# Optimization experiments

Measured on AMD Instinct MI355X. Metric: run time of the kernel, lower is better.

## Reference

```python
import jax, jax.numpy as jnp
import numpy as np

N_NODES = 100000
N_EDGES = 800000
F_IN = 16
F_OUT = 16
NB = 4          # basis terms per coordinate dimension (dims=[4,4] -> K=16)
OUTPUT_SCALING = 1.0 / 128.0


def hat_basis(u, n):
    """'linear' RBF: hat functions on [-1,1]. u: [E] -> [E, n]."""
    centers = jnp.linspace(-1.0, 1.0, n, dtype=u.dtype)   # [n]
    width = 2.0 / (n - 1)
    return jnp.maximum(0.0, 1.0 - jnp.abs(u[:, None] - centers[None, :]) / width)


def setup_inputs() -> dict:
    key = jax.random.key(0)
    k1, k2, k3, k4, k5 = jax.random.split(key, 5)
    x = jax.random.normal(k1, (N_NODES, F_IN), dtype=jnp.float32)
    edge_attr = jax.random.normal(k2, (N_EDGES, 2), dtype=jnp.float32) * 0.7
    # conv weight tensor: [K, F_in, F_out], xavier-ish scale with gain 1/sqrt(34)
    W = jax.random.normal(k3, (NB * NB, F_IN, F_OUT), dtype=jnp.float32) * (
        (1.0 / np.sqrt(34.0)) * np.sqrt(2.0 / (F_IN + F_OUT)))
    edge_index_i = jax.random.randint(k4, (N_EDGES,), 0, N_NODES, dtype=jnp.int64)
    edge_index_j = jax.random.randint(k5, (N_EDGES,), 0, N_NODES, dtype=jnp.int64)
    return {"x": x, "edge_attr": edge_attr, "W": W,
            "edge_index_i": edge_index_i, "edge_index_j": edge_index_j}


def reference(x, edge_attr, W, edge_index_i, edge_index_j):
    # --- process(): centerIgnore mask, clamp, cartesian mapping (identity) ---
    mask = edge_index_i != edge_index_j                      # [E]
    mapped = jnp.clip(edge_attr, -1.0, 1.0)                  # [E, 2]

    # --- tensor-product 'linear' basis evaluation: [E, K] ---
    bx = hat_basis(mapped[:, 0], NB)                         # [E, NB]
    by = hat_basis(mapped[:, 1], NB)                         # [E, NB]
    basis = (bx[:, :, None] * by[:, None, :]).reshape(mapped.shape[0], NB * NB)

    # --- continuous conv: gather, per-edge basis-weighted linear, scatter ---
    xj = x[edge_index_j]                                     # [E, F_in] gather
    u = jnp.einsum('ei,kio->eko', xj, W)                     # [E, K, F_out]
    msg = jnp.einsum('ek,eko->eo', basis, u)                 # [E, F_out]
    msg = jnp.where(mask[:, None], msg, jnp.zeros((), msg.dtype))
    out = jax.ops.segment_sum(msg, edge_index_i, num_segments=x.shape[0])
    return out * OUTPUT_SCALING
```

## Files before the change

kernel.cpp:

```cpp
#include <hip/hip_runtime.h>

#define N_NODES 100000
#define N_EDGES 800000
#define NBY    ((N_NODES + 255) / 256)
#define HBLK   ((N_EDGES + 255) / 256)
#define OVF_CAP 65536
#define GA     1000
#define CHUNK  800
#define NBINS  512
#define NPB    196
#define CAPB   2048
#define GB_T   1024
#define CURSTRIDE 64

__device__ __forceinline__ unsigned short f2bf(float f) {
    union { float f; unsigned u; } v; v.f = f;
    unsigned u = v.u;
    return (unsigned short)((u + 0x7FFFu + ((u >> 16) & 1u)) >> 16);
}
__device__ __forceinline__ float bflo(unsigned u) {
    union { unsigned u; float f; } v; v.u = u << 16; return v.f;
}
__device__ __forceinline__ float bfhi(unsigned u) {
    union { unsigned u; float f; } v; v.u = u & 0xFFFF0000u; return v.f;
}

__global__ __launch_bounds__(256) void bucket_build(
    const float* __restrict__ edge_attr,
    const int* __restrict__ ei, const int* __restrict__ ej,
    int* __restrict__ cursor, uint2* __restrict__ bkt,
    int* __restrict__ ovfCnt, int* __restrict__ ovf) {
    const int b = blockIdx.x;
    __shared__ int hist[NBINS];
    __shared__ unsigned rawA[CHUNK];
    __shared__ unsigned rawB[CHUNK];
    __shared__ short rawBin[CHUNK];
    const int tid = threadIdx.x;
    for (int k = tid; k < NBINS; k += 256) hist[k] = 0;
    __syncthreads();
    const int base = b * CHUNK;

    for (int i = 0; i < CHUNK; i += 256) {
        const int j = i + tid;
        if (j >= CHUNK) continue;
        const int e = base + j;
        short binS = -1;
        if (e < N_EDGES) {
            const int di = ei[e];
            const int sj = ej[e];
            if (di != sj) {
                const float2 ea = ((const float2*)edge_attr)[e];
                float ux = fminf(fmaxf(ea.x, -1.f), 1.f);
                float uy = fminf(fmaxf(ea.y, -1.f), 1.f);
                float tx = (ux + 1.f) * 1.5f;
                float ty = (uy + 1.f) * 1.5f;
                int kx0 = min((int)tx, 2);
                int ky0 = min((int)ty, 2);
                float fx = tx - (float)kx0;
                float fy = ty - (float)ky0;
                unsigned fx12 = (unsigned)(fx * 4095.f + 0.5f);
                unsigned fy12 = (unsigned)(fy * 4095.f + 0.5f);
                const int bin = di / NPB;
                const unsigned local = (unsigned)(di - bin * NPB);
                rawA[j] = (unsigned)(sj * 512 + (kx0 * 4 + ky0) * 32);
                rawB[j] = fx12 | (fy12 << 12) | (local << 24);
                binS = (short)bin;
                atomicAdd(&hist[bin], 1);
            }
        }
        rawBin[j] = binS;
    }
    __syncthreads();

    for (int k = tid; k < NBINS; k += 256) {
        const int c = hist[k];
        int g = 0;
        if (c > 0) g = atomicAdd(&cursor[k * CURSTRIDE], c);
        hist[k] = k * CAPB + g;
    }
    __syncthreads();

    for (int i = 0; i < CHUNK; i += 256) {
        const int j = i + tid;
        if (j >= CHUNK) continue;
        const int bin = rawBin[j];
        if (bin < 0) continue;
        const int s = atomicAdd(&hist[bin], 1);
        if (s - bin * CAPB < CAPB) {
            bkt[s] = make_uint2(rawA[j], rawB[j]);
        } else {
            const int o = atomicAdd(ovfCnt, 1);
            if (o < OVF_CAP) ovf[o] = base + j;
        }
    }
}

__global__ __launch_bounds__(GB_T) void gather_conv(
    const int* __restrict__ cursor, const uint2* __restrict__ bkt,
    const float* __restrict__ x, const float* __restrict__ W,
    float* __restrict__ out,
    const int* __restrict__ ovfCnt, const int* __restrict__ ovf,
    const float* __restrict__ edge_attr, const int* __restrict__ ei,
    const int* __restrict__ ej) {
    const int bin = blockIdx.x;
    const int tid = threadIdx.x;
    __shared__ uint2 sorted[CAPB];
    __shared__ __align__(16) char u_buf[20480];
    __shared__ int h[NPB];
    __shared__ int st[NPB], en[NPB], cur[NPB];
    __shared__ float tile[NPB * 16];
    uint2* raw = (uint2*)u_buf;
    float* Wl  = (float*)u_buf;

    for (int j = tid; j < NPB; j += GB_T) h[j] = 0;
    __syncthreads();

    const int cnt = min(cursor[bin * CURSTRIDE], CAPB);
    const int pad = (cnt + NPB <= CAPB) ? 1 : 0;
    const uint2* rb = bkt + (size_t)bin * CAPB;

    for (int p = tid; p < cnt; p += GB_T) {
        uint2 r = rb[p];
        raw[p] = r;
        atomicAdd(&h[r.y >> 24], 1);
    }
    __syncthreads();

    int c0 = (tid < NPB) ? h[tid] : 0;
    for (int off = 1; off < NPB; off <<= 1) {
        int tmp = 0;
        if (tid < NPB && tid >= off) tmp = h[tid - off];
        __syncthreads();
        if (tid < NPB) h[tid] += tmp;
        __syncthreads();
    }
    if (tid < NPB) {
        const int sh = tid * pad;
        en[tid]  = h[tid] + sh;
        st[tid]  = h[tid] - c0 + sh;
        cur[tid] = h[tid] - c0 + sh;
    }
    __syncthreads();

    for (int p = tid; p < cnt; p += GB_T) {
        uint2 r = raw[p];
        int pos = atomicAdd(&cur[r.y >> 24], 1);
        sorted[pos] = r;
    }
    __syncthreads();

    {
        float4 w = ((const float4*)W)[tid];
        const int k = tid >> 6, i = (tid >> 2) & 15, o4 = tid & 3;
        *(float4*)&Wl[k * 320 + i * 20 + o4 * 4] = w;
    }
    __syncthreads();

    const float U = 1.f / 4095.f;
    const float S = 1.f / 128.f;
    if (tid < 4 * NPB) {
        const int node = tid >> 2;
        const int q4 = tid & 3;
        float t[16][4];
#pragma unroll
        for (int k = 0; k < 16; ++k)
#pragma unroll
            for (int i = 0; i < 4; ++i) t[k][i] = 0.f;

        const int lo = st[node], hi2 = en[node];
        uint2 m = make_uint2(0u, 0u);
        float4 xv = make_float4(0.f, 0.f, 0.f, 0.f);
        if (lo < hi2) {
            m = sorted[lo];
            xv = ((const float4*)x)[(m.x >> 9) * 4 + q4];
        }
        for (int idx = lo; idx < hi2; ++idx) {
            const uint2 mc = m;
            const float4 xc = xv;
            if (idx + 1 < hi2) {
                m = sorted[idx + 1];
                xv = ((const float4*)x)[(m.x >> 9) * 4 + q4];
            }
            const unsigned koff = (mc.x >> 5) & 15u;
            const int kx0 = (int)(koff >> 2);
            const int ky0 = (int)(koff & 3u);
            const float fx = (float)(mc.y & 0xFFFu) * U;
            const float fy = (float)((mc.y >> 12) & 0xFFFu) * U;
            float wx[4], wy[4];
#pragma unroll
            for (int a = 0; a < 4; ++a) {
                wx[a] = (a == kx0) ? (1.f - fx) : ((a == kx0 + 1) ? fx : 0.f);
                wy[a] = (a == ky0) ? (1.f - fy) : ((a == ky0 + 1) ? fy : 0.f);
            }
            const float xr[4] = {xc.x, xc.y, xc.z, xc.w};
#pragma unroll
            for (int kx = 0; kx < 4; ++kx)
#pragma unroll
                for (int ky = 0; ky < 4; ++ky) {
                    const float w = wx[kx] * wy[ky];
#pragma unroll
                    for (int i = 0; i < 4; ++i)
                        t[kx * 4 + ky][i] = fmaf(w, xr[i], t[kx * 4 + ky][i]);
                }
        }

        float po[16];
#pragma unroll
        for (int o = 0; o < 16; ++o) po[o] = 0.f;
#pragma unroll
        for (int k = 0; k < 16; ++k)
#pragma unroll
            for (int il = 0; il < 4; ++il) {
                const float tv = t[k][il];
                const float4* wr = (const float4*)&Wl[k * 320 + (q4 * 4 + il) * 20];
                const float4 w0 = wr[0], w1 = wr[1], w2 = wr[2], w3 = wr[3];
                po[0]  = fmaf(tv, w0.x, po[0]);  po[1]  = fmaf(tv, w0.y, po[1]);
                po[2]  = fmaf(tv, w0.z, po[2]);  po[3]  = fmaf(tv, w0.w, po[3]);
                po[4]  = fmaf(tv, w1.x, po[4]);  po[5]  = fmaf(tv, w1.y, po[5]);
                po[6]  = fmaf(tv, w1.z, po[6]);  po[7]  = fmaf(tv, w1.w, po[7]);
                po[8]  = fmaf(tv, w2.x, po[8]);  po[9]  = fmaf(tv, w2.y, po[9]);
                po[10] = fmaf(tv, w2.z, po[10]); po[11] = fmaf(tv, w2.w, po[11]);
                po[12] = fmaf(tv, w3.x, po[12]); po[13] = fmaf(tv, w3.y, po[13]);
                po[14] = fmaf(tv, w3.z, po[14]); po[15] = fmaf(tv, w3.w, po[15]);
            }

#pragma unroll
        for (int o = 0; o < 16; ++o) {
            po[o] += __shfl_xor(po[o], 1);
            po[o] += __shfl_xor(po[o], 2);
        }
        if (q4 == 0) {
            float* tr = &tile[node * 16];
#pragma unroll
            for (int o = 0; o < 16; ++o) tr[o] = po[o] * S;
        }
    }
    __syncthreads();

    const int m = min(*ovfCnt, OVF_CAP);
    if (m > 0) {
        const int nlo = bin * NPB;
        const int nhi = min(nlo + NPB, N_NODES);
        for (int i = tid; i < m; i += GB_T) {
            const int e = ovf[i];
            const int di = ei[e];
            if (di < nlo || di >= nhi) continue;
            const int sj = ej[e];
            const float2 ea = ((const float2*)edge_attr)[e];
            float ux = fminf(fmaxf(ea.x, -1.f), 1.f);
            float uy = fminf(fmaxf(ea.y, -1.f), 1.f);
            float tx = (ux + 1.f) * 1.5f, ty = (uy + 1.f) * 1.5f;
            int kx0 = min((int)tx, 2), ky0 = min((int)ty, 2);
            float fx = tx - (float)kx0, fy = ty - (float)ky0;
            float wgt[4] = {(1.f-fx)*(1.f-fy)*S, (1.f-fx)*fy*S, fx*(1.f-fy)*S, fx*fy*S};
            int kidx[4] = {kx0*4+ky0, kx0*4+ky0+1, (kx0+1)*4+ky0, (kx0+1)*4+ky0+1};
            const float* xj = x + (size_t)sj * 16;
            float msg[16];
#pragma unroll
            for (int o = 0; o < 16; ++o) msg[o] = 0.f;
#pragma unroll
            for (int p = 0; p < 4; ++p) {
                const float* wk = Wl + kidx[p] * 320;
                for (int ii = 0; ii < 16; ++ii) {
                    float xw = xj[ii] * wgt[p];
#pragma unroll
                    for (int o = 0; o < 16; ++o)
                        msg[o] = fmaf(xw, wk[ii * 20 + o], msg[o]);
                }
            }
            float* tr = &tile[(di - nlo) * 16];
#pragma unroll
            for (int o = 0; o < 16; ++o) atomicAdd(tr + o, msg[o]);
        }
        __syncthreads();
    }

    const int base = bin * NPB * 16;
    const int lim = N_NODES * 16 - base;
    for (int j = tid; j < NPB * 16; j += GB_T)
        if (j < lim) out[base + j] = tile[j];
}

__global__ __launch_bounds__(256) void y_only_kernel(
    const float* __restrict__ x, const float* __restrict__ W,
    unsigned short* __restrict__ Y) {
    const int n = blockIdx.x * 256 + threadIdx.x;
    const int kbase = blockIdx.y * 4;
    if (n >= N_NODES) return;
    const float4* xv = (const float4*)(x + n * 16);
    float4 a = xv[0], b = xv[1], c = xv[2], d = xv[3];
    float xr[16] = {a.x,a.y,a.z,a.w, b.x,b.y,b.z,b.w,
                    c.x,c.y,c.z,c.w, d.x,d.y,d.z,d.w};
    float acc[4][16];
#pragma unroll
    for (int kk = 0; kk < 4; ++kk)
#pragma unroll
        for (int o = 0; o < 16; ++o) acc[kk][o] = 0.f;
#pragma unroll
    for (int i = 0; i < 16; ++i)
#pragma unroll
        for (int kk = 0; kk < 4; ++kk) {
            const float* wrow = W + ((kbase + kk) * 256 + i * 16);
#pragma unroll
            for (int o = 0; o < 16; ++o)
                acc[kk][o] = fmaf(xr[i], wrow[o], acc[kk][o]);
        }
    unsigned short* dst = Y + (size_t)n * 256 + kbase * 16;
#pragma unroll
    for (int kk = 0; kk < 4; ++kk) {
        unsigned pk[8];
#pragma unroll
        for (int q = 0; q < 8; ++q)
            pk[q] = (unsigned)f2bf(acc[kk][2*q]) | ((unsigned)f2bf(acc[kk][2*q+1]) << 16);
        uint4* p = (uint4*)(dst + kk * 16);
        p[0] = make_uint4(pk[0], pk[1], pk[2], pk[3]);
        p[1] = make_uint4(pk[4], pk[5], pk[6], pk[7]);
    }
}

__global__ __launch_bounds__(256) void edge_kernel(
    const float* __restrict__ edge_attr, const int* __restrict__ ei,
    const int* __restrict__ ej, const unsigned short* __restrict__ Y,
    float* __restrict__ out) {
    const int e = blockIdx.x * 256 + threadIdx.x;
    if (e >= N_EDGES) return;
    const int di = ei[e];
    const int sj = ej[e];
    const float2 ea = ((const float2*)edge_attr)[e];
    if (di == sj) return;
    float ux = fminf(fmaxf(ea.x, -1.f), 1.f);
    float uy = fminf(fmaxf(ea.y, -1.f), 1.f);
    float tx = (ux + 1.f) * 1.5f;
    float ty = (uy + 1.f) * 1.5f;
    int kx0 = min((int)tx, 2);
    int ky0 = min((int)ty, 2);
    float fx = tx - (float)kx0;
    float fy = ty - (float)ky0;
    const float S = 1.f / 128.f;
    float w00 = (1.f - fx) * (1.f - fy) * S;
    float w01 = (1.f - fx) * fy * S;
    float w10 = fx * (1.f - fy) * S;
    float w11 = fx * fy * S;
    const unsigned short* base = Y + (size_t)sj * 256 + (kx0 * 4 + ky0) * 16;
    const uint4* pA = (const uint4*)base;
    const uint4* pB = (const uint4*)(base + 64);
    uint4 a0 = pA[0], a1 = pA[1], a2 = pA[2], a3 = pA[3];
    uint4 b0 = pB[0], b1 = pB[1], b2 = pB[2], b3 = pB[3];
    unsigned ra0[8] = {a0.x,a0.y,a0.z,a0.w, a1.x,a1.y,a1.z,a1.w};
    unsigned ra1[8] = {a2.x,a2.y,a2.z,a2.w, a3.x,a3.y,a3.z,a3.w};
    unsigned rb0[8] = {b0.x,b0.y,b0.z,b0.w, b1.x,b1.y,b1.z,b1.w};
    unsigned rb1[8] = {b2.x,b2.y,b2.z,b2.w, b3.x,b3.y,b3.z,b3.w};
    float* o16 = out + (size_t)di * 16;
#pragma unroll
    for (int q = 0; q < 8; ++q) {
        float m0 = bflo(ra0[q]) * w00 + bflo(ra1[q]) * w01
                 + bflo(rb0[q]) * w10 + bflo(rb1[q]) * w11;
        float m1 = bfhi(ra0[q]) * w00 + bfhi(ra1[q]) * w01
                 + bfhi(rb0[q]) * w10 + bfhi(rb1[q]) * w11;
        atomicAdd(o16 + 2 * q, m0);
        atomicAdd(o16 + 2 * q + 1, m1);
    }
}

__global__ __launch_bounds__(256) void edge_direct(
    const float* __restrict__ x, const float* __restrict__ edge_attr,
    const float* __restrict__ W, const int* __restrict__ ei,
    const int* __restrict__ ej, float* __restrict__ out) {
    const int e = blockIdx.x * 256 + threadIdx.x;
    if (e >= N_EDGES) return;
    const int di = ei[e];
    const int sj = ej[e];
    const float2 ea = ((const float2*)edge_attr)[e];
    if (di == sj) return;
    float ux = fminf(fmaxf(ea.x, -1.f), 1.f);
    float uy = fminf(fmaxf(ea.y, -1.f), 1.f);
    float tx = (ux + 1.f) * 1.5f, ty = (uy + 1.f) * 1.5f;
    int kx0 = min((int)tx, 2), ky0 = min((int)ty, 2);
    float fx = tx - (float)kx0, fy = ty - (float)ky0;
    const float S = 1.f / 128.f;
    float wgt[4] = {(1.f-fx)*(1.f-fy)*S, (1.f-fx)*fy*S, fx*(1.f-fy)*S, fx*fy*S};
    int kidx[4] = {kx0*4+ky0, kx0*4+ky0+1, (kx0+1)*4+ky0, (kx0+1)*4+ky0+1};
    const float* xj = x + (size_t)sj * 16;
    float xr[16];
#pragma unroll
    for (int i = 0; i < 16; ++i) xr[i] = xj[i];
    float msg[16];
#pragma unroll
    for (int o = 0; o < 16; ++o) msg[o] = 0.f;
#pragma unroll
    for (int p = 0; p < 4; ++p) {
        const float* wk = W + kidx[p] * 256;
#pragma unroll
        for (int i = 0; i < 16; ++i) {
            float xw = xr[i] * wgt[p];
#pragma unroll
            for (int o = 0; o < 16; ++o)
                msg[o] = fmaf(xw, wk[i * 16 + o], msg[o]);
        }
    }
    float* o16 = out + (size_t)di * 16;
#pragma unroll
    for (int o = 0; o < 16; ++o) atomicAdd(o16 + o, msg[o]);
}

extern "C" void kernel_launch(void* const* d_in, const int* in_sizes, int n_in,
                              void* d_out, int out_size, void* d_ws, size_t ws_size,
                              hipStream_t stream) {
    const float* x         = (const float*)d_in[0];
    const float* edge_attr = (const float*)d_in[1];
    const float* W         = (const float*)d_in[2];
    const int*   ei        = (const int*)d_in[3];
    const int*   ej        = (const int*)d_in[4];
    float* out = (float*)d_out;
    char* ws = (char*)d_ws;

    const size_t oCur    = 0;
    const size_t oOvfCnt = oCur + (size_t)NBINS * CURSTRIDE * 4;
    const size_t oOvf    = oOvfCnt + 16;
    const size_t oBkt    = oOvf + (size_t)OVF_CAP * 4;
    const size_t total   = oBkt + (size_t)NBINS * CAPB * 8;

    if (ws_size >= total) {
        int*   cursor = (int*)(ws + oCur);
        int*   ovfCnt = (int*)(ws + oOvfCnt);
        int*   ovf    = (int*)(ws + oOvf);
        uint2* bkt    = (uint2*)(ws + oBkt);

        hipMemsetAsync(cursor, 0, (size_t)NBINS * CURSTRIDE * 4 + 16, stream);
        bucket_build<<<GA, 256, 0, stream>>>(
            edge_attr, ei, ej, cursor, bkt, ovfCnt, ovf);
        gather_conv<<<NBINS, GB_T, 0, stream>>>(
            cursor, bkt, x, W, out, ovfCnt, ovf, edge_attr, ei, ej);
        return;
    }

    const size_t yBytes = (size_t)N_NODES * 512;
    if (ws_size >= yBytes) {
        hipMemsetAsync(d_out, 0, (size_t)out_size * sizeof(float), stream);
        unsigned short* Y = (unsigned short*)d_ws;
        dim3 gA(NBY, 4);
        y_only_kernel<<<gA, 256, 0, stream>>>(x, W, Y);
        edge_kernel<<<HBLK, 256, 0, stream>>>(edge_attr, ei, ej, Y, out);
    } else {
        hipMemsetAsync(d_out, 0, (size_t)out_size * sizeof(float), stream);
        edge_direct<<<HBLK, 256, 0, stream>>>(x, edge_attr, W, ei, ej, out);
    }
}
```

Baseline: 139.0 us.

## Use wavefront shuffle scan for bin prefix sum and retune binning grid

The per-bin node histogram prefix sum now uses a 64-lane shuffle-up scan plus a small per-wave total array, replacing a Hillis-Steele scan that issued two block-wide barriers per step across a 1024-thread block. This is meant to cut barrier overhead in the gather_conv prologue. Separately, the binning kernel's grid is shrunk from 1000 to 250 blocks while each block's chunk grows from 800 to 3200 edges. That may reduce launch and atomic contention but also lowers parallelism in that stage.

Result: faster. 130.3 us (-6.2%).

```diff
diff --git a/kernel.cpp b/kernel.cpp
--- a/kernel.cpp
+++ b/kernel.cpp
@@ -5,8 +5,8 @@
 #define NBY    ((N_NODES + 255) / 256)
 #define HBLK   ((N_EDGES + 255) / 256)
 #define OVF_CAP 65536
-#define GA     1000
-#define CHUNK  800
+#define GA     250
+#define CHUNK  3200
 #define NBINS  512
 #define NPB    196
 #define CAPB   2048
@@ -108,6 +108,7 @@
     __shared__ __align__(16) char u_buf[20480];
     __shared__ int h[NPB];
     __shared__ int st[NPB], en[NPB], cur[NPB];
+    __shared__ int wsum[4];
     __shared__ float tile[NPB * 16];
     uint2* raw = (uint2*)u_buf;
     float* Wl  = (float*)u_buf;
@@ -126,19 +127,30 @@
     }
     __syncthreads();
 
-    int c0 = (tid < NPB) ? h[tid] : 0;
-    for (int off = 1; off < NPB; off <<= 1) {
-        int tmp = 0;
-        if (tid < NPB && tid >= off) tmp = h[tid - off];
-        __syncthreads();
-        if (tid < NPB) h[tid] += tmp;
-        __syncthreads();
-    }
+    const int lane = tid & 63;
+    const int wid  = tid >> 6;
+    int c0 = 0, v = 0;
+    if (tid < 256) {
+        c0 = (tid < NPB) ? h[tid] : 0;
+        v = c0;
+#pragma unroll
+        for (int off = 1; off < 64; off <<= 1) {
+            int u = __shfl_up(v, off);
+            if (lane >= off) v += u;
+        }
+        if (lane == 63) wsum[wid] = v;
+    }
+    __syncthreads();
     if (tid < NPB) {
+        int pfx = 0;
+#pragma unroll
+        for (int w = 0; w < 4; ++w)
+            if (w < wid) pfx += wsum[w];
+        const int incl = v + pfx;
         const int sh = tid * pad;
-        en[tid]  = h[tid] + sh;
-        st[tid]  = h[tid] - c0 + sh;
-        cur[tid] = h[tid] - c0 + sh;
+        en[tid]  = incl + sh;
+        st[tid]  = incl - c0 + sh;
+        cur[tid] = incl - c0 + sh;
     }
     __syncthreads();
 
```
